# Kernel tuning notes

Measured on AMD Instinct MI355X. Metric: run time of the kernel, lower is better.

Reference implementation:

```python
import jax, jax.numpy as jnp
import numpy as np

K = 20
LN_EPS = 1e-5
NEG_SLOPE = 0.2


def _knn(x, k):
    # x: (B, C, N) -> idx (B, N, k) of k nearest neighbors (incl. self)
    xx = jnp.sum(x * x, axis=1)                      # (B, N)
    inner = jnp.einsum('bcn,bcm->bnm', x, x)         # (B, N, N)
    pd = -xx[:, :, None] + 2.0 * inner - xx[:, None, :]  # -||xi-xj||^2
    return jax.lax.top_k(pd, k)[1]


def _layernorm(h, g, b):
    m = jnp.mean(h, axis=-1, keepdims=True)
    v = jnp.var(h, axis=-1, keepdims=True)
    return (h - m) * jax.lax.rsqrt(v + LN_EPS) * g + b


def _edge_conv(x, k, W, g, b):
    # x: (B, C, N); W: (Cout, 2C) 1x1 conv; returns (B, Cout, N)
    idx = _knn(x, k)                                 # (B, N, k)
    xt = jnp.transpose(x, (0, 2, 1))                 # (B, N, C)
    nbr = jax.vmap(lambda f, i: f[i])(xt, idx)       # (B, N, k, C)
    ctr = xt[:, :, None, :]                          # (B, N, 1, C)
    comb = jnp.concatenate([nbr - ctr, jnp.broadcast_to(ctr, nbr.shape)], axis=-1)
    h = jnp.einsum('oc,bnkc->bnko', W, comb)         # (B, N, k, Cout)
    h = _layernorm(h, g, b)
    h = jnp.where(h >= 0, h, NEG_SLOPE * h)          # LeakyReLU(0.2)
    return jnp.transpose(jnp.max(h, axis=2), (0, 2, 1))


def _normalize(x):
    # x: (B, 3, N) -> center and scale to unit max radius
    c = jnp.mean(x, axis=2, keepdims=True)
    xc = x - c
    md = jnp.max(jnp.sqrt(jnp.sum(xc * xc, axis=1)), axis=1)[:, None, None]
    return xc / (md + 1e-8)


def setup_inputs() -> dict:
    key = jax.random.key(0)
    ks = jax.random.split(key, 13)
    f32 = jnp.float32
    x = jax.random.normal(ks[0], (4, 3, 4096), dtype=f32)
    def conv_w(k_, cout, cin):
        return jax.random.normal(k_, (cout, cin), dtype=f32) * (1.0 / np.sqrt(cin))
    return {
        'x': x,
        'W1': conv_w(ks[1], 16, 6),  'g1': jnp.ones((16,), f32), 'b1': jnp.zeros((16,), f32),
        'W2': conv_w(ks[2], 16, 32), 'g2': jnp.ones((16,), f32), 'b2': jnp.zeros((16,), f32),
        'W3': conv_w(ks[3], 32, 32), 'g3': jnp.ones((32,), f32), 'b3': jnp.zeros((32,), f32),
        'W4': conv_w(ks[4], 64, 64), 'g4': jnp.ones((64,), f32), 'b4': jnp.zeros((64,), f32),
    }


def reference(x, W1, g1, b1, W2, g2, b2, W3, g3, b3, W4, g4, b4):
    xn = _normalize(x)
    x1 = _edge_conv(xn, K, W1, g1, b1)   # (B, 16, N)
    x2 = _edge_conv(x1, K, W2, g2, b2)   # (B, 16, N)
    x3 = _edge_conv(x2, K, W3, g3, b3)   # (B, 32, N)
    x4 = _edge_conv(x3, K, W4, g4, b4)   # (B, 64, N)
    x_cat = jnp.concatenate([x1, x2, x3, x4], axis=1)  # (B, 128, N)
    return jnp.max(x_cat, axis=-1)                     # (B, 128)
```

## Files before the change

### kernel.cpp

```cpp
#include <hip/hip_runtime.h>

#define K_NN 20
#define LN_EPS 1e-5f
#define NEG_SLOPE 0.2f
#define BUFSZ 15
#define ARRSZ 32

__device__ __forceinline__ unsigned ordf(float f){
  unsigned u = __float_as_uint(f);
  return u ^ (((unsigned)((int)u >> 31)) | 0x80000000u);
}
__device__ __forceinline__ float unordf(unsigned u){
  unsigned m = ((int)u < 0) ? 0x80000000u : 0xFFFFFFFFu;
  return __uint_as_float(u ^ m);
}

__device__ __forceinline__ void ce_desc(unsigned long long &a, unsigned long long &b){
  unsigned long long mx = a>b ? a : b;
  unsigned long long mn = a>b ? b : a;
  a = mx; b = mn;
}

__device__ __forceinline__ void sort16_desc(unsigned long long (&v)[16]){
  #pragma unroll
  for (int k=2;k<=16;k<<=1){
    #pragma unroll
    for (int j=k>>1;j>0;j>>=1){
      #pragma unroll
      for (int i=0;i<16;++i){
        int l = i ^ j;
        if (l > i){
          if ((i & k) == 0) ce_desc(v[i], v[l]);
          else              ce_desc(v[l], v[i]);
        }
      }
    }
  }
}

__device__ __forceinline__ void bmerge32_desc(unsigned long long (&v)[32]){
  #pragma unroll
  for (int d=16; d>0; d>>=1){
    #pragma unroll
    for (int i=0;i<32;++i){
      if ((i & d) == 0) ce_desc(v[i], v[i|d]);
    }
  }
}

__global__ __launch_bounds__(1024) void normalize_kernel(const float* __restrict__ x,
                                                         float* __restrict__ xn,
                                                         float* __restrict__ xxo, int N){
  __shared__ float red[1024];
  __shared__ float ms[4];
  const int b = blockIdx.x;
  const int t = threadIdx.x;
  const float* xb = x + (size_t)b*3*N;
  float s0=0.f,s1=0.f,s2=0.f;
  for (int n=t;n<N;n+=1024){ s0+=xb[n]; s1+=xb[N+n]; s2+=xb[2*N+n]; }
  red[t]=s0; __syncthreads();
  for(int o=512;o>0;o>>=1){ if(t<o) red[t]+=red[t+o]; __syncthreads(); }
  if(!t) ms[0]=red[0]/(float)N; __syncthreads();
  red[t]=s1; __syncthreads();
  for(int o=512;o>0;o>>=1){ if(t<o) red[t]+=red[t+o]; __syncthreads(); }
  if(!t) ms[1]=red[0]/(float)N; __syncthreads();
  red[t]=s2; __syncthreads();
  for(int o=512;o>0;o>>=1){ if(t<o) red[t]+=red[t+o]; __syncthreads(); }
  if(!t) ms[2]=red[0]/(float)N; __syncthreads();
  const float m0=ms[0], m1=ms[1], m2=ms[2];
  float mx=0.f;
  for (int n=t;n<N;n+=1024){
    float a=xb[n]-m0, c1=xb[N+n]-m1, c2=xb[2*N+n]-m2;
    mx = fmaxf(mx, a*a+c1*c1+c2*c2);
  }
  red[t]=mx; __syncthreads();
  for(int o=512;o>0;o>>=1){ if(t<o) red[t]=fmaxf(red[t],red[t+o]); __syncthreads(); }
  if(!t) ms[3]=sqrtf(red[0])+1e-8f; __syncthreads();
  const float md=ms[3];
  for (int n=t;n<N;n+=1024){
    float a=xb[n]-m0, c1=xb[N+n]-m1, c2=xb[2*N+n]-m2;
    float4 v; v.x=a/md; v.y=c1/md; v.z=c2/md; v.w=0.f;
    reinterpret_cast<float4*>(xn)[(size_t)b*N+n]=v;
    float s=0.f;
    s=fmaf(v.x,v.x,s); s=fmaf(v.y,v.y,s); s=fmaf(v.z,v.z,s); s=fmaf(v.w,v.w,s);
    xxo[b*N+n]=s;
  }
}

template<int CP4>
__global__ __launch_bounds__(512,4) void knn_kernel(const float* __restrict__ feat,
                                                    const float* __restrict__ xx,
                                                    unsigned* __restrict__ pd32,
                                                    unsigned short* __restrict__ pi16,
                                                    int N){
  __shared__ unsigned long long sbuf[BUFSZ*512];
  const int ng = N>>6;
  const int s  = blockIdx.x & 1;
  const int gi = blockIdx.x >> 1;
  const int b  = gi / ng;
  const int n0 = (gi % ng) << 6;
  const int tid = threadIdx.x;
  const int lane = tid & 63;
  const int w = __builtin_amdgcn_readfirstlane(tid >> 6);
  const int bN = b*N;
  const int n = n0 + lane;
  const float4* fb = reinterpret_cast<const float4*>(feat);
  float4 own[CP4];
  #pragma unroll
  for (int i=0;i<CP4;++i) own[i] = fb[(size_t)(bN+n)*CP4 + i];

  auto pdof = [&](int m)->float{
    const float4* cp = fb + (size_t)(bN+m)*CP4;
    float d0=0.f, d1=0.f;
    #pragma unroll
    for (int i=0;i<CP4;++i){
      float4 c = cp[i];
      d0 = fmaf(own[i].x,c.x,d0);
      d1 = fmaf(own[i].y,c.y,d1);
      d0 = fmaf(own[i].z,c.z,d0);
      d1 = fmaf(own[i].w,c.w,d1);
    }
    return fmaf(2.f, d0+d1, -xx[bN+m]);
  };

  const int m0 = s*(N>>1) + w*(N>>4);

  unsigned long long arr[ARRSZ];
  float thresh;
  int cnt = 0;

  {
    unsigned long long bv1[16], bv2[16];
    #pragma unroll
    for (int j=0;j<16;++j){
      float pd = pdof(m0+j);
      bv1[j] = ((unsigned long long)ordf(pd)<<32) | (unsigned)((m0+j) ^ 0xFFFF);
    }
    sort16_desc(bv1);
    #pragma unroll
    for (int j=0;j<16;++j){
      float pd = pdof(m0+16+j);
      bv2[j] = ((unsigned long long)ordf(pd)<<32) | (unsigned)((m0+16+j) ^ 0xFFFF);
    }
    sort16_desc(bv2);
    #pragma unroll
    for (int i=0;i<ARRSZ;++i) arr[i] = (i<16) ? bv1[i] : bv2[31-i];
    bmerge32_desc(arr);
    thresh = unordf((unsigned)(arr[K_NN-1]>>32));
  }

  auto do_flush = [&](){
    unsigned long long bv[16];
    #pragma unroll
    for (int q=0;q<16;++q){
      unsigned long long v = (q<BUFSZ) ? sbuf[q*512 + tid] : 0ull;
      bv[q] = (q < cnt) ? v : 0ull;
    }
    sort16_desc(bv);
    #pragma unroll
    for (int i=16;i<32;++i){
      unsigned long long t2 = bv[31-i];
      arr[i] = arr[i] > t2 ? arr[i] : t2;
    }
    bmerge32_desc(arr);
    thresh = unordf((unsigned)(arr[K_NN-1]>>32));
    cnt = 0;
  };

  constexpr int C = (CP4==1) ? 8 : 4;
  const int nchunks = ((N>>4) - 32) / C;
  for (int ch=0; ch<nchunks; ++ch){
    const int mc = m0 + 32 + ch*C;
    float pdv[C];
    #pragma unroll
    for (int j=0;j<C;++j) pdv[j] = pdof(mc+j);
    #pragma unroll
    for (int j=0;j<C;++j){
      if (pdv[j] >= thresh){
        sbuf[cnt*512 + tid] =
          ((unsigned long long)ordf(pdv[j])<<32) | (unsigned)((mc+j) ^ 0xFFFF);
        ++cnt;
      }
    }
    if (__ballot(cnt >= BUFSZ-C)) do_flush();
  }
  if (__ballot(cnt > 0)) do_flush();

  __syncthreads();
  unsigned* lkh = (unsigned*)sbuf;
  unsigned short* lki = (unsigned short*)(((char*)sbuf)+40960);
  #pragma unroll
  for (int i=0;i<K_NN;++i){
    lkh[((w*K_NN+i)<<6)+lane] = (unsigned)(arr[i]>>32);
    lki[((w*K_NN+i)<<6)+lane] = (unsigned short)(arr[i]&0xFFFFu);
  }
  __syncthreads();
  if (tid < 64){
    const int l = tid;
    unsigned long long heads[8];
    #pragma unroll
    for (int j=0;j<8;++j){
      int q0=((j*K_NN)<<6)+l;
      heads[j]=((unsigned long long)lkh[q0]<<16)|(unsigned long long)lki[q0];
    }
    unsigned long long pk=0ull;
    const size_t pbase = ((size_t)(bN+n0+l)*2 + s)*K_NN;
    for (int kk=0;kk<K_NN;++kk){
      unsigned long long best=heads[0]; int bj=0;
      #pragma unroll
      for (int j=1;j<8;++j){ bool gg=heads[j]>best; best=gg?heads[j]:best; bj=gg?j:bj; }
      pd32[pbase+kk] = (unsigned)(best>>16);
      pi16[pbase+kk] = (unsigned short)(best & 0xFFFFu);
      unsigned pos = (unsigned)((pk>>(bj*5))&0x1Ful)+1u;
      pk += (1ull<<(bj*5));
      unsigned long long nv = 0ull;
      if (pos<K_NN){
        int q1=((bj*K_NN+(int)pos)<<6)+l;
        nv=((unsigned long long)lkh[q1]<<16)|(unsigned long long)lki[q1];
      }
      #pragma unroll
      for (int j=0;j<8;++j) heads[j]=(j==bj)?nv:heads[j];
    }
  }
}

template<int CIN,int CP4,int O>
__global__ __launch_bounds__(256) void merge_ctr_kernel(const unsigned* __restrict__ pd32,
                                                        const unsigned short* __restrict__ pi16,
                                                        int* __restrict__ idx_out,
                                                        const float* __restrict__ feat,
                                                        const float* __restrict__ W,
                                                        float* __restrict__ h0, int total){
  int i = blockIdx.x*256 + threadIdx.x;
  if (i>=total) return;
  {
    const unsigned* d0 = pd32 + (size_t)i*2*K_NN;
    const unsigned short* i0 = pi16 + (size_t)i*2*K_NN;
    const unsigned* d1 = d0 + K_NN;
    const unsigned short* i1 = i0 + K_NN;
    int a=0, c=0;
    int* op = idx_out + (size_t)i*K_NN;
    #pragma unroll 4
    for (int k=0;k<K_NN;++k){
      unsigned long long k0 = ((unsigned long long)d0[a]<<16) | i0[a];
      unsigned long long k1 = ((unsigned long long)d1[c]<<16) | i1[c];
      bool t = k0 > k1;
      unsigned long long best = t ? k0 : k1;
      op[k] = (int)(((unsigned)best & 0xFFFFu) ^ 0xFFFFu);
      a += t; c += !t;
    }
  }
  {
    const float4* p = reinterpret_cast<const float4*>(feat)+(size_t)i*CP4;
    float c[CP4*4];
    #pragma unroll
    for (int j=0;j<CP4;++j){
      float4 v=p[j];
      c[4*j+0]=v.x; c[4*j+1]=v.y; c[4*j+2]=v.z; c[4*j+3]=v.w;
    }
    float* hp = h0 + (size_t)i*O;
    #pragma unroll
    for (int o=0;o<O;++o){
      const float* wr = W + o*(2*CIN) + CIN;
      float a=0.f;
      #pragma unroll
      for (int cc=0;cc<CIN;++cc) a=fmaf(wr[cc],c[cc],a);
      hp[o]=a;
    }
  }
}

template<int CIN,int CP4,int O>
__global__ __launch_bounds__(320) void edge_kernel(const float* __restrict__ feat,
      const int* __restrict__ knn_idx, const float* __restrict__ h0,
      const float* __restrict__ W, const float* __restrict__ g, const float* __restrict__ bb,
      float* __restrict__ outf, float* __restrict__ xxo, int N){
  __shared__ unsigned ob[16*O];
  const int t = threadIdx.x;
  const int p = t/K_NN, k = t - p*K_NN;
  const int b = blockIdx.y;
  const int n = blockIdx.x*16 + p;
  const int bN = b*N;
  for (int v=t; v<16*O; v+=320) ob[v]=0u;
  __syncthreads();
  const int m = knn_idx[(size_t)(bN+n)*K_NN + k];
  const float4* fb = reinterpret_cast<const float4*>(feat);
  float d[CP4*4];
  #pragma unroll
  for (int j=0;j<CP4;++j){
    float4 a = fb[(size_t)(bN+m)*CP4+j];
    float4 c = fb[(size_t)(bN+n)*CP4+j];
    d[4*j+0]=a.x-c.x; d[4*j+1]=a.y-c.y; d[4*j+2]=a.z-c.z; d[4*j+3]=a.w-c.w;
  }
  float h[O];
  const float4* hp = reinterpret_cast<const float4*>(h0 + (size_t)(bN+n)*O);
  #pragma unroll
  for (int j=0;j<O/4;++j){ float4 v=hp[j]; h[4*j]=v.x; h[4*j+1]=v.y; h[4*j+2]=v.z; h[4*j+3]=v.w; }
  #pragma unroll
  for (int o=0;o<O;++o){
    const float* wr = W + o*(2*CIN);
    float a=h[o];
    #pragma unroll
    for (int cc=0;cc<CIN;++cc) a=fmaf(wr[cc],d[cc],a);
    h[o]=a;
  }
  float mean=0.f;
  #pragma unroll
  for (int o=0;o<O;++o) mean+=h[o];
  mean *= (1.f/(float)O);
  float var=0.f;
  #pragma unroll
  for (int o=0;o<O;++o){ float dd=h[o]-mean; var=fmaf(dd,dd,var); }
  var *= (1.f/(float)O);
  const float r = rsqrtf(var+LN_EPS);
  #pragma unroll
  for (int o=0;o<O;++o){
    float hv = (h[o]-mean)*r*g[o]+bb[o];
    hv = (hv>=0.f)? hv : NEG_SLOPE*hv;
    atomicMax(&ob[p*O+o], ordf(hv));
  }
  __syncthreads();
  for (int v=t; v<16*O; v+=320){
    int pp=v/O, oo=v-pp*O;
    outf[(size_t)(bN+blockIdx.x*16+pp)*O+oo]=unordf(ob[v]);
  }
  if (t < 16){
    float s=0.f;
    for (int oo=0;oo<O;++oo){
      float f = unordf(ob[t*O+oo]);
      s = fmaf(f,f,s);
    }
    xxo[bN + blockIdx.x*16 + t] = s;
  }
}

__global__ __launch_bounds__(256) void final_max_kernel(const float* __restrict__ x1,
    const float* __restrict__ x2, const float* __restrict__ x3, const float* __restrict__ x4,
    float* __restrict__ out, int N){
  __shared__ float red[256];
  const int L=blockIdx.x, b=blockIdx.y;
  const float* f; int O, off;
  if (L==0){f=x1;O=16;off=0;}
  else if (L==1){f=x2;O=16;off=16;}
  else if (L==2){f=x3;O=32;off=32;}
  else {f=x4;O=64;off=64;}
  const int t=threadIdx.x;
  const int c=t%O, s=t/O, S=256/O;
  float acc=-3.402823466e38f;
  for (int n=s;n<N;n+=S) acc=fmaxf(acc, f[(size_t)(b*N+n)*O+c]);
  red[t]=acc; __syncthreads();
  if (t<O){
    float a=red[t];
    for (int ss=1;ss<S;++ss) a=fmaxf(a,red[ss*O+t]);
    out[b*128+off+t]=a;
  }
}

extern "C" void kernel_launch(void* const* d_in, const int* in_sizes, int n_in,
                              void* d_out, int out_size, void* d_ws, size_t ws_size,
                              hipStream_t stream){
  const float* x  = (const float*)d_in[0];
  const float* W1 = (const float*)d_in[1];  const float* g1=(const float*)d_in[2];  const float* b1=(const float*)d_in[3];
  const float* W2 = (const float*)d_in[4];  const float* g2=(const float*)d_in[5];  const float* b2=(const float*)d_in[6];
  const float* W3 = (const float*)d_in[7];  const float* g3=(const float*)d_in[8];  const float* b3=(const float*)d_in[9];
  const float* W4 = (const float*)d_in[10]; const float* g4=(const float*)d_in[11]; const float* b4=(const float*)d_in[12];
  float* out=(float*)d_out;
  const int B=4;
  const int N=in_sizes[0]/(3*B);
  const int BN=B*N;

  char* ws=(char*)d_ws;
  size_t off=0;
  auto alloc=[&](size_t bytes)->void*{ void* p=ws+off; off=(off+bytes+255)&~(size_t)255; return p; };
  float* xn =(float*)alloc((size_t)BN*4*4);
  float* x1 =(float*)alloc((size_t)BN*16*4);
  float* x2 =(float*)alloc((size_t)BN*16*4);
  float* x3 =(float*)alloc((size_t)BN*32*4);
  float* x4 =(float*)alloc((size_t)BN*64*4);
  float* xxb=(float*)alloc((size_t)BN*4);
  int*   knn=(int*)  alloc((size_t)BN*K_NN*4);
  float* h0 =(float*)alloc((size_t)BN*64*4);
  unsigned*       pd32=(unsigned*)      alloc((size_t)BN*2*K_NN*4);
  unsigned short* pi16=(unsigned short*)alloc((size_t)BN*2*K_NN*2);

  dim3 pb((BN+255)/256), tb(256);
  dim3 kb(B*(N/64)*2), kt(512);
  dim3 eb(N/16,B), et(320);

  normalize_kernel<<<dim3(B),dim3(1024),0,stream>>>(x,xn,xxb,N);

  knn_kernel<1><<<kb,kt,0,stream>>>(xn,xxb,pd32,pi16,N);
  merge_ctr_kernel<3,1,16><<<pb,tb,0,stream>>>(pd32,pi16,knn,xn,W1,h0,BN);
  edge_kernel<3,1,16><<<eb,et,0,stream>>>(xn,knn,h0,W1,g1,b1,x1,xxb,N);

  knn_kernel<4><<<kb,kt,0,stream>>>(x1,xxb,pd32,pi16,N);
  merge_ctr_kernel<16,4,16><<<pb,tb,0,stream>>>(pd32,pi16,knn,x1,W2,h0,BN);
  edge_kernel<16,4,16><<<eb,et,0,stream>>>(x1,knn,h0,W2,g2,b2,x2,xxb,N);

  knn_kernel<4><<<kb,kt,0,stream>>>(x2,xxb,pd32,pi16,N);
  merge_ctr_kernel<16,4,32><<<pb,tb,0,stream>>>(pd32,pi16,knn,x2,W3,h0,BN);
  edge_kernel<16,4,32><<<eb,et,0,stream>>>(x2,knn,h0,W3,g3,b3,x3,xxb,N);

  knn_kernel<8><<<kb,kt,0,stream>>>(x3,xxb,pd32,pi16,N);
  merge_ctr_kernel<32,8,64><<<pb,tb,0,stream>>>(pd32,pi16,knn,x3,W4,h0,BN);
  edge_kernel<32,8,64><<<eb,et,0,stream>>>(x3,knn,h0,W4,g4,b4,x4,xxb,N);

  final_max_kernel<<<dim3(4,B),dim3(256),0,stream>>>(x1,x2,x3,x4,out,N);
}
```

Measured before the change: 1.004 ms.

## Restructure kNN into 16 candidate slices staged in LDS with 16-way merge

The kNN kernel now gives each block 512 query points against one 256-candidate slice, whose coordinates and norms are staged in shared memory, instead of each wave streaming candidates from global memory. The overflow buffer stores floats plus 8-bit local indices rather than 64-bit keys, which shrinks LDS use, and the in-block 8-way merge is removed. Each thread writes its own top-20 per slice, and the merge kernel does a 16-way head merge. The trade-off is 8x larger partial-result traffic and a heavier, less coalesced merge step.

```diff
diff --git a/kernel.cpp b/kernel.cpp
--- a/kernel.cpp
+++ b/kernel.cpp
@@ -3,8 +3,9 @@
 #define K_NN 20
 #define LN_EPS 1e-5f
 #define NEG_SLOPE 0.2f
-#define BUFSZ 15
+#define BUFSZ 12
 #define ARRSZ 32
+#define NSLICE 16
 
 __device__ __forceinline__ unsigned ordf(float f){
   unsigned u = __float_as_uint(f);
@@ -91,26 +92,37 @@
 __global__ __launch_bounds__(512,4) void knn_kernel(const float* __restrict__ feat,
                                                     const float* __restrict__ xx,
                                                     unsigned* __restrict__ pd32,
-                                                    unsigned short* __restrict__ pi16,
-                                                    int N){
-  __shared__ unsigned long long sbuf[BUFSZ*512];
-  const int ng = N>>6;
-  const int s  = blockIdx.x & 1;
-  const int gi = blockIdx.x >> 1;
-  const int b  = gi / ng;
-  const int n0 = (gi % ng) << 6;
+                                                    unsigned char* __restrict__ pi8,
+                                                    int N, int BN){
+  constexpr int STAGEB = CP4*256*16;
+  __shared__ char smem[STAGEB + 1024 + BUFSZ*512*4 + BUFSZ*512];
+  float4* scoord = (float4*)smem;
+  float*  sxx    = (float*)(smem + STAGEB);
+  float*  pdbuf  = (float*)(smem + STAGEB + 1024);
+  unsigned char* idxbuf = (unsigned char*)(smem + STAGEB + 1024 + BUFSZ*512*4);
+
+  const int gpb = N >> 9;
+  const int gq  = blockIdx.x >> 4;
+  const int s   = blockIdx.x & (NSLICE-1);
+  const int b   = gq / gpb;
+  const int n0  = (gq - b*gpb) << 9;
   const int tid = threadIdx.x;
-  const int lane = tid & 63;
-  const int w = __builtin_amdgcn_readfirstlane(tid >> 6);
-  const int bN = b*N;
-  const int n = n0 + lane;
+  const int bN  = b*N;
+  const int m0  = s << 8;
   const float4* fb = reinterpret_cast<const float4*>(feat);
+
+  {
+    const float4* src = fb + (size_t)(bN + m0)*CP4;
+    for (int j = tid; j < 256*CP4; j += 512) scoord[j] = src[j];
+    if (tid < 256) sxx[tid] = xx[bN + m0 + tid];
+  }
   float4 own[CP4];
   #pragma unroll
-  for (int i=0;i<CP4;++i) own[i] = fb[(size_t)(bN+n)*CP4 + i];
-
-  auto pdof = [&](int m)->float{
-    const float4* cp = fb + (size_t)(bN+m)*CP4;
+  for (int i=0;i<CP4;++i) own[i] = fb[(size_t)(bN + n0 + tid)*CP4 + i];
+  __syncthreads();
+
+  auto pdof = [&](int j)->float{
+    const float4* cp = scoord + j*CP4;
     float d0=0.f, d1=0.f;
     #pragma unroll
     for (int i=0;i<CP4;++i){
@@ -120,10 +132,8 @@
       d0 = fmaf(own[i].z,c.z,d0);
       d1 = fmaf(own[i].w,c.w,d1);
     }
-    return fmaf(2.f, d0+d1, -xx[bN+m]);
+    return fmaf(2.f, d0+d1, -sxx[j]);
   };
-
-  const int m0 = s*(N>>1) + w*(N>>4);
 
   unsigned long long arr[ARRSZ];
   float thresh;
@@ -133,13 +143,13 @@
     unsigned long long bv1[16], bv2[16];
     #pragma unroll
     for (int j=0;j<16;++j){
-      float pd = pdof(m0+j);
+      float pd = pdof(j);
       bv1[j] = ((unsigned long long)ordf(pd)<<32) | (unsigned)((m0+j) ^ 0xFFFF);
     }
     sort16_desc(bv1);
     #pragma unroll
     for (int j=0;j<16;++j){
-      float pd = pdof(m0+16+j);
+      float pd = pdof(16+j);
       bv2[j] = ((unsigned long long)ordf(pd)<<32) | (unsigned)((m0+16+j) ^ 0xFFFF);
     }
     sort16_desc(bv2);
@@ -153,8 +163,13 @@
     unsigned long long bv[16];
     #pragma unroll
     for (int q=0;q<16;++q){
-      unsigned long long v = (q<BUFSZ) ? sbuf[q*512 + tid] : 0ull;
-      bv[q] = (q < cnt) ? v : 0ull;
+      unsigned long long key = 0ull;
+      if (q<BUFSZ){
+        float pd = pdbuf[q*512 + tid];
+        unsigned j8 = idxbuf[q*512 + tid];
+        key = ((unsigned long long)ordf(pd)<<32) | (unsigned)((m0+(int)j8) ^ 0xFFFF);
+      }
+      bv[q] = (q < cnt) ? key : 0ull;
     }
     sort16_desc(bv);
     #pragma unroll
@@ -167,18 +182,17 @@
     cnt = 0;
   };
 
-  constexpr int C = (CP4==1) ? 8 : 4;
-  const int nchunks = ((N>>4) - 32) / C;
-  for (int ch=0; ch<nchunks; ++ch){
-    const int mc = m0 + 32 + ch*C;
+  constexpr int C = 4;
+  for (int ch=0; ch<(256-32)/C; ++ch){
+    const int jc = 32 + ch*C;
     float pdv[C];
     #pragma unroll
-    for (int j=0;j<C;++j) pdv[j] = pdof(mc+j);
+    for (int j=0;j<C;++j) pdv[j] = pdof(jc+j);
     #pragma unroll
     for (int j=0;j<C;++j){
       if (pdv[j] >= thresh){
-        sbuf[cnt*512 + tid] =
-          ((unsigned long long)ordf(pdv[j])<<32) | (unsigned)((mc+j) ^ 0xFFFF);
+        pdbuf[cnt*512 + tid]  = pdv[j];
+        idxbuf[cnt*512 + tid] = (unsigned char)(jc+j);
         ++cnt;
       }
     }
@@ -186,47 +200,22 @@
   }
   if (__ballot(cnt > 0)) do_flush();
 
-  __syncthreads();
-  unsigned* lkh = (unsigned*)sbuf;
-  unsigned short* lki = (unsigned short*)(((char*)sbuf)+40960);
-  #pragma unroll
-  for (int i=0;i<K_NN;++i){
-    lkh[((w*K_NN+i)<<6)+lane] = (unsigned)(arr[i]>>32);
-    lki[((w*K_NN+i)<<6)+lane] = (unsigned short)(arr[i]&0xFFFFu);
-  }
-  __syncthreads();
-  if (tid < 64){
-    const int l = tid;
-    unsigned long long heads[8];
-    #pragma unroll
-    for (int j=0;j<8;++j){
-      int q0=((j*K_NN)<<6)+l;
-      heads[j]=((unsigned long long)lkh[q0]<<16)|(unsigned long long)lki[q0];
-    }
-    unsigned long long pk=0ull;
-    const size_t pbase = ((size_t)(bN+n0+l)*2 + s)*K_NN;
-    for (int kk=0;kk<K_NN;++kk){
-      unsigned long long best=heads[0]; int bj=0;
-      #pragma unroll
-      for (int j=1;j<8;++j){ bool gg=heads[j]>best; best=gg?heads[j]:best; bj=gg?j:bj; }
-      pd32[pbase+kk] = (unsigned)(best>>16);
-      pi16[pbase+kk] = (unsigned short)(best & 0xFFFFu);
-      unsigned pos = (unsigned)((pk>>(bj*5))&0x1Ful)+1u;
-      pk += (1ull<<(bj*5));
-      unsigned long long nv = 0ull;
-      if (pos<K_NN){
-        int q1=((bj*K_NN+(int)pos)<<6)+l;
-        nv=((unsigned long long)lkh[q1]<<16)|(unsigned long long)lki[q1];
-      }
-      #pragma unroll
-      for (int j=0;j<8;++j) heads[j]=(j==bj)?nv:heads[j];
+  {
+    const size_t p = (size_t)(bN + n0 + tid);
+    unsigned*       od = pd32 + ((size_t)s*BN + p)*K_NN;
+    unsigned char*  oi = pi8  + ((size_t)s*BN + p)*K_NN;
+    #pragma unroll
+    for (int k=0;k<K_NN;++k){
+      od[k] = (unsigned)(arr[k]>>32);
+      unsigned m = ((unsigned)arr[k] ^ 0xFFFFu) & 0xFFFFu;
+      oi[k] = (unsigned char)(m & 255u);
     }
   }
 }
 
 template<int CIN,int CP4,int O>
 __global__ __launch_bounds__(256) void merge_ctr_kernel(const unsigned* __restrict__ pd32,
-                                                        const unsigned short* __restrict__ pi16,
+                                                        const unsigned char* __restrict__ pi8,
                                                         int* __restrict__ idx_out,
                                                         const float* __restrict__ feat,
                                                         const float* __restrict__ W,
@@ -234,20 +223,29 @@
   int i = blockIdx.x*256 + threadIdx.x;
   if (i>=total) return;
   {
-    const unsigned* d0 = pd32 + (size_t)i*2*K_NN;
-    const unsigned short* i0 = pi16 + (size_t)i*2*K_NN;
-    const unsigned* d1 = d0 + K_NN;
-    const unsigned short* i1 = i0 + K_NN;
-    int a=0, c=0;
+    auto keyat = [&](int s, int pos)->unsigned long long{
+      unsigned d = pd32[((size_t)s*total + i)*K_NN + pos];
+      unsigned j8 = pi8[((size_t)s*total + i)*K_NN + pos];
+      unsigned m = (unsigned)(s*256) + j8;
+      return ((unsigned long long)d<<16) | (unsigned)((m ^ 0xFFFF) & 0xFFFFu);
+    };
+    unsigned long long heads[NSLICE];
+    #pragma unroll
+    for (int j=0;j<NSLICE;++j) heads[j] = keyat(j, 0);
+    unsigned long long pk0=0ull, pk1=0ull;
     int* op = idx_out + (size_t)i*K_NN;
-    #pragma unroll 4
     for (int k=0;k<K_NN;++k){
-      unsigned long long k0 = ((unsigned long long)d0[a]<<16) | i0[a];
-      unsigned long long k1 = ((unsigned long long)d1[c]<<16) | i1[c];
-      bool t = k0 > k1;
-      unsigned long long best = t ? k0 : k1;
+      unsigned long long best=heads[0]; int bj=0;
+      #pragma unroll
+      for (int j=1;j<NSLICE;++j){ bool gg=heads[j]>best; best=gg?heads[j]:best; bj=gg?j:bj; }
       op[k] = (int)(((unsigned)best & 0xFFFFu) ^ 0xFFFFu);
-      a += t; c += !t;
+      unsigned pos;
+      if (bj < 8){ pos = (unsigned)((pk0>>(bj*8))&0xFFull)+1u; pk0 += (1ull<<(bj*8)); }
+      else       { pos = (unsigned)((pk1>>((bj-8)*8))&0xFFull)+1u; pk1 += (1ull<<((bj-8)*8)); }
+      unsigned long long nv = 0ull;
+      if (pos < K_NN) nv = keyat(bj, (int)pos);
+      #pragma unroll
+      for (int j=0;j<NSLICE;++j) heads[j]=(j==bj)?nv:heads[j];
     }
   }
   {
@@ -380,29 +378,29 @@
   float* xxb=(float*)alloc((size_t)BN*4);
   int*   knn=(int*)  alloc((size_t)BN*K_NN*4);
   float* h0 =(float*)alloc((size_t)BN*64*4);
-  unsigned*       pd32=(unsigned*)      alloc((size_t)BN*2*K_NN*4);
-  unsigned short* pi16=(unsigned short*)alloc((size_t)BN*2*K_NN*2);
+  unsigned*      pd32=(unsigned*)     alloc((size_t)NSLICE*BN*K_NN*4);
+  unsigned char* pi8 =(unsigned char*)alloc((size_t)NSLICE*BN*K_NN);
 
   dim3 pb((BN+255)/256), tb(256);
-  dim3 kb(B*(N/64)*2), kt(512);
+  dim3 kb((BN/512)*NSLICE), kt(512);
   dim3 eb(N/16,B), et(320);
 
   normalize_kernel<<<dim3(B),dim3(1024),0,stream>>>(x,xn,xxb,N);
 
-  knn_kernel<1><<<kb,kt,0,stream>>>(xn,xxb,pd32,pi16,N);
-  merge_ctr_kernel<3,1,16><<<pb,tb,0,stream>>>(pd32,pi16,knn,xn,W1,h0,BN);
+  knn_kernel<1><<<kb,kt,0,stream>>>(xn,xxb,pd32,pi8,N,BN);
+  merge_ctr_kernel<3,1,16><<<pb,tb,0,stream>>>(pd32,pi8,knn,xn,W1,h0,BN);
   edge_kernel<3,1,16><<<eb,et,0,stream>>>(xn,knn,h0,W1,g1,b1,x1,xxb,N);
 
-  knn_kernel<4><<<kb,kt,0,stream>>>(x1,xxb,pd32,pi16,N);
-  merge_ctr_kernel<16,4,16><<<pb,tb,0,stream>>>(pd32,pi16,knn,x1,W2,h0,BN);
+  knn_kernel<4><<<kb,kt,0,stream>>>(x1,xxb,pd32,pi8,N,BN);
+  merge_ctr_kernel<16,4,16><<<pb,tb,0,stream>>>(pd32,pi8,knn,x1,W2,h0,BN);
   edge_kernel<16,4,16><<<eb,et,0,stream>>>(x1,knn,h0,W2,g2,b2,x2,xxb,N);
 
-  knn_kernel<4><<<kb,kt,0,stream>>>(x2,xxb,pd32,pi16,N);
-  merge_ctr_kernel<16,4,32><<<pb,tb,0,stream>>>(pd32,pi16,knn,x2,W3,h0,BN);
+  knn_kernel<4><<<kb,kt,0,stream>>>(x2,xxb,pd32,pi8,N,BN);
+  merge_ctr_kernel<16,4,32><<<pb,tb,0,stream>>>(pd32,pi8,knn,x2,W3,h0,BN);
   edge_kernel<16,4,32><<<eb,et,0,stream>>>(x2,knn,h0,W3,g3,b3,x3,xxb,N);
 
-  knn_kernel<8><<<kb,kt,0,stream>>>(x3,xxb,pd32,pi16,N);
-  merge_ctr_kernel<32,8,64><<<pb,tb,0,stream>>>(pd32,pi16,knn,x3,W4,h0,BN);
+  knn_kernel<8><<<kb,kt,0,stream>>>(x3,xxb,pd32,pi8,N,BN);
+  merge_ctr_kernel<32,8,64><<<pb,tb,0,stream>>>(pd32,pi8,knn,x3,W4,h0,BN);
   edge_kernel<32,8,64><<<eb,et,0,stream>>>(x3,knn,h0,W4,g4,b4,x4,xxb,N);
 
   final_max_kernel<<<dim3(4,B),dim3(256),0,stream>>>(x1,x2,x3,x4,out,N);
```

New measurement: 1.402 ms. 39.6% more time.
